# Performance work log

Measured on AMD Instinct MI355X. Metric: run time of the kernel, lower is better.

Reference implementation:

```python
import jax, jax.numpy as jnp
import numpy as np

NUM_HEADS = 32
NUM_KV_HEADS = 8
HEAD_DIM = 128
HIDDEN = 4096
ROPE_THETA = 10000.0
RMS_EPS = 1e-6


def setup_inputs() -> dict:
    key = jax.random.key(0)
    k1, k2, k3 = jax.random.split(key, 3)
    T = 2048
    qkv_out = (NUM_HEADS + 2 * NUM_KV_HEADS) * HEAD_DIM  # 6144
    return {
        "positions": jnp.arange(T, dtype=jnp.int64),
        "hidden_states": jax.random.normal(k1, (T, HIDDEN), dtype=jnp.float32),
        "wqkv": jax.random.normal(k2, (qkv_out, HIDDEN), dtype=jnp.float32) * 0.02,
        "wo": jax.random.normal(k3, (HIDDEN, NUM_HEADS * HEAD_DIM), dtype=jnp.float32) * 0.02,
        "q_norm_w": jnp.ones((HEAD_DIM,), dtype=jnp.float32),
        "k_norm_w": jnp.ones((HEAD_DIM,), dtype=jnp.float32),
    }


def _rms_norm(x, w):
    # per-head RMSNorm over last dim, computed in fp32 (matches Dots1RMSNorm)
    xf = x.astype(jnp.float32)
    var = jnp.mean(xf * xf, axis=-1, keepdims=True)
    return (w * (xf * jax.lax.rsqrt(var + RMS_EPS))).astype(x.dtype)


def _rope(x, positions):
    # NeoX-style rotary: rotate halves. x: [T, H, D]
    half = HEAD_DIM // 2
    inv_freq = 1.0 / (ROPE_THETA ** (jnp.arange(0, half, dtype=jnp.float32) / half))
    ang = positions.astype(jnp.float32)[:, None] * inv_freq  # [T, half]
    cos = jnp.cos(ang)[:, None, :]  # [T,1,half]
    sin = jnp.sin(ang)[:, None, :]
    x1, x2 = x[..., :half], x[..., half:]
    return jnp.concatenate([x1 * cos - x2 * sin, x2 * cos + x1 * sin], axis=-1)


def reference(positions, hidden_states, wqkv, wo, q_norm_w, k_norm_w):
    T = hidden_states.shape[0]
    q_size = NUM_HEADS * HEAD_DIM
    kv_size = NUM_KV_HEADS * HEAD_DIM
    qkv = hidden_states @ wqkv.T  # [T, q_size + 2*kv_size]
    q = qkv[:, :q_size].reshape(T, NUM_HEADS, HEAD_DIM)
    k = qkv[:, q_size:q_size + kv_size].reshape(T, NUM_KV_HEADS, HEAD_DIM)
    v = qkv[:, q_size + kv_size:].reshape(T, NUM_KV_HEADS, HEAD_DIM)

    q = _rms_norm(q, q_norm_w)
    k = _rms_norm(k, k_norm_w)
    q = _rope(q, positions)
    k = _rope(k, positions)

    # GQA: expand kv heads to query heads (group of 4)
    group = NUM_HEADS // NUM_KV_HEADS
    k = jnp.repeat(k, group, axis=1)  # [T, H, D]
    v = jnp.repeat(v, group, axis=1)

    scale = HEAD_DIM ** -0.5
    scores = jnp.einsum('thd,shd->hts', q, k) * scale  # [H, T, T]
    causal = positions[:, None] >= positions[None, :]
    scores = jnp.where(causal[None, :, :], scores, jnp.finfo(scores.dtype).min)
    probs = jax.nn.softmax(scores, axis=-1)
    attn = jnp.einsum('hts,shd->thd', probs, v)  # [T, H, D]
    out = attn.reshape(T, NUM_HEADS * HEAD_DIM) @ wo.T  # [T, HIDDEN]
    return out
```

## Files before the change

kernel.cpp:

```cpp
#include <hip/hip_runtime.h>


#define T_SEQ 2048
#define HID   4096
#define NH    32
#define NKVH  8
#define HD    128
#define QKVN  6144
#define QSZ   4096
#define QKN   5120

typedef unsigned short u16;
typedef __attribute__((ext_vector_type(8))) short short8;
typedef __attribute__((ext_vector_type(4))) float floatx4;

__device__ __forceinline__ float bf2f(u16 u) {
  union { unsigned int i; float f; } c; c.i = ((unsigned int)u) << 16; return c.f;
}
__device__ __forceinline__ u16 f2bf(float f) {
  union { float f; unsigned int i; } c; c.f = f;
  unsigned int u = c.i;
  return (u16)((u + 0x7FFFu + ((u >> 16) & 1u)) >> 16);
}
__device__ __forceinline__ floatx4 mfma16(short8 a, short8 b, floatx4 c) {
  return __builtin_amdgcn_mfma_f32_16x16x32_bf16(a, b, c, 0, 0, 0);
}

#define GLD16(g, l) __builtin_amdgcn_global_load_lds( \
    (__attribute__((address_space(1))) unsigned int*)(g), \
    (__attribute__((address_space(3))) unsigned int*)(l), 16, 0, 0)

__global__ __launch_bounds__(256) void cvt3_kernel(
    const float* __restrict__ s0, const float* __restrict__ s1,
    const float* __restrict__ s2, u16* __restrict__ d0, u16* __restrict__ d1,
    u16* __restrict__ d2, int n0, int n1, int n2) {
  int total = n0 + n1 + n2;
  int stride = gridDim.x * 256;
  for (int i = blockIdx.x * 256 + threadIdx.x; i < total; i += stride) {
    const float* s; u16* d; int j = i;
    if (j < n0)           { s = s0; d = d0; }
    else if (j < n0 + n1) { j -= n0; s = s1; d = d1; }
    else                  { j -= n0 + n1; s = s2; d = d2; }
    float4 a = ((const float4*)s)[2 * j];
    float4 b = ((const float4*)s)[2 * j + 1];
    union { ushort u[8]; uint4 v; } o;
    o.u[0] = f2bf(a.x); o.u[1] = f2bf(a.y); o.u[2] = f2bf(a.z); o.u[3] = f2bf(a.w);
    o.u[4] = f2bf(b.x); o.u[5] = f2bf(b.y); o.u[6] = f2bf(b.z); o.u[7] = f2bf(b.w);
    ((uint4*)d)[j] = o.v;
  }
}

template <int MODE>
__global__ __launch_bounds__(256, 2) void gemm_bt(const u16* __restrict__ A,
    const u16* __restrict__ B, void* __restrict__ Cv, u16* __restrict__ VT,
    int mtiles, int K, int ldC) {
  __shared__ __attribute__((aligned(16))) u16 As[128 * 64];
  __shared__ __attribute__((aligned(16))) u16 Bs[128 * 64];
  const int tid = threadIdx.x;
  const int wave = tid >> 6, lane = tid & 63;
  const int lq = lane >> 4, lc = lane & 15;
  const int wm = wave >> 1, wn = wave & 1;
  const int id = ((int)blockIdx.x & 7) * ((int)gridDim.x >> 3) + ((int)blockIdx.x >> 3);
  const int by = id % mtiles, bx = id / mtiles;
  const int m0 = by * 128, n0 = bx * 128;

  floatx4 acc[4][4];
#pragma unroll
  for (int i = 0; i < 4; ++i)
#pragma unroll
    for (int j = 0; j < 4; ++j) acc[i][j] = {0.f, 0.f, 0.f, 0.f};

  int arow[4], brow[4];
#pragma unroll
  for (int i = 0; i < 4; ++i) {
    arow[i] = wm * 64 + i * 16 + lc;
    brow[i] = wn * 64 + i * 16 + lc;
  }

  const u16* asrc[4]; const u16* bsrc[4];
#pragma unroll
  for (int r = 0; r < 4; ++r) {
    int L = r * 256 + tid;
    int mm = L >> 3;
    int cc = (L & 7) ^ (mm & 7);
    asrc[r] = A + (size_t)(m0 + mm) * K + cc * 8;
    bsrc[r] = B + (size_t)(n0 + mm) * K + cc * 8;
  }

  for (int k0 = 0; k0 < K; k0 += 64) {
#pragma unroll
    for (int r = 0; r < 4; ++r) {
      GLD16(asrc[r] + k0, As + (r * 256 + wave * 64) * 8);
      GLD16(bsrc[r] + k0, Bs + (r * 256 + wave * 64) * 8);
    }
    __syncthreads();
#pragma unroll
    for (int kb = 0; kb < 2; ++kb) {
      short8 af[4], bfr[4];
#pragma unroll
      for (int mi = 0; mi < 4; ++mi)
        af[mi] = *(const short8*)&As[arow[mi] * 64 + (((kb * 4 + lq) ^ (arow[mi] & 7)) * 8)];
#pragma unroll
      for (int ni = 0; ni < 4; ++ni)
        bfr[ni] = *(const short8*)&Bs[brow[ni] * 64 + (((kb * 4 + lq) ^ (brow[ni] & 7)) * 8)];
#pragma unroll
      for (int mi = 0; mi < 4; ++mi)
#pragma unroll
        for (int ni = 0; ni < 4; ++ni)
          acc[mi][ni] = mfma16(af[mi], bfr[ni], acc[mi][ni]);
    }
    __syncthreads();
  }

  if (MODE == 1 && n0 >= 5120) {
#pragma unroll
    for (int mi = 0; mi < 4; ++mi) {
      int row = m0 + wm * 64 + mi * 16 + lq * 4;
#pragma unroll
      for (int ni = 0; ni < 4; ++ni) {
        int rel = n0 + wn * 64 + ni * 16 + lc - 5120;
        ushort4 u;
        u.x = f2bf(acc[mi][ni][0]); u.y = f2bf(acc[mi][ni][1]);
        u.z = f2bf(acc[mi][ni][2]); u.w = f2bf(acc[mi][ni][3]);
        *(ushort4*)&VT[(size_t)rel * T_SEQ + row] = u;
      }
    }
  } else {
#pragma unroll
    for (int mi = 0; mi < 4; ++mi) {
      int row = m0 + wm * 64 + mi * 16 + lq * 4;
#pragma unroll
      for (int ni = 0; ni < 4; ++ni) {
        int col = n0 + wn * 64 + ni * 16 + lc;
#pragma unroll
        for (int r = 0; r < 4; ++r) {
          if (MODE == 1)
            ((u16*)Cv)[(size_t)(row + r) * ldC + col] = f2bf(acc[mi][ni][r]);
          else
            ((float*)Cv)[(size_t)(row + r) * ldC + col] = acc[mi][ni][r];
        }
      }
    }
  }
}

__global__ __launch_bounds__(256) void norm_rope_kernel(const u16* __restrict__ qk,
    const float* __restrict__ qw, const float* __restrict__ kw,
    u16* __restrict__ Qo, u16* __restrict__ Ko) {
  const int t = blockIdx.x;
  const int w = threadIdx.x >> 6;
  const int l = threadIdx.x & 63;
  const float inv = exp2f((float)l * -0.20762050593045158f);
  float s, c;
  __sincosf((float)t * inv, &s, &c);
  const float qwl = qw[l], qwh = qw[l + 64];
  const float kwl = kw[l], kwh = kw[l + 64];
  const u16* row = qk + (size_t)t * QKN;
#pragma unroll 2
  for (int hs = w; hs < NH + NKVH; hs += 4) {
    const bool isq = hs < NH;
    const u16* src = row + hs * HD;
    float x1 = bf2f(src[l]);
    float x2 = bf2f(src[l + 64]);
    float ss = x1 * x1 + x2 * x2;
#pragma unroll
    for (int m = 1; m < 64; m <<= 1) ss += __shfl_xor(ss, m);
    float rstd = rsqrtf(ss * (1.0f / HD) + 1e-6f);
    float n1 = x1 * rstd * (isq ? qwl : kwl);
    float n2 = x2 * rstd * (isq ? qwh : kwh);
    float o1 = n1 * c - n2 * s;
    float o2 = n2 * c + n1 * s;
    if (isq) {
      o1 *= 0.08838834764831845f; o2 *= 0.08838834764831845f;
      u16* dst = Qo + ((size_t)hs * T_SEQ + t) * HD;
      dst[l] = f2bf(o1); dst[l + 64] = f2bf(o2);
    } else {
      u16* dst = Ko + ((size_t)(hs - NH) * T_SEQ + t) * HD;
      dst[l] = f2bf(o1); dst[l + 64] = f2bf(o2);
    }
  }
}

__global__ __launch_bounds__(256, 2) void attn_kernel(const u16* __restrict__ Qg,
    const u16* __restrict__ Kg, const u16* __restrict__ VTg, u16* __restrict__ Og) {
  __shared__ __attribute__((aligned(16))) u16 Ks[8192];
  __shared__ __attribute__((aligned(16))) u16 Vs[2][8192];
  __shared__ __attribute__((aligned(16))) u16 Ps[8192];

  const int bid = blockIdx.x;
  const int h = bid & 31;
  const int qq = bid >> 5;
  const int qt = (qq < 8) ? (15 - qq) : (qq - 8);
  const int kvh = h >> 2;
  const int tid = threadIdx.x;
  const int wave = tid >> 6, lane = tid & 63;
  const int lq = lane >> 4, lc = lane & 15;

  const u16* kbase[4];
  const u16* vbase[4];
#pragma unroll
  for (int i = 0; i < 4; ++i) {
    int L = i * 256 + tid;
    int s = L >> 4, cp = L & 15;
    kbase[i] = Kg + ((size_t)kvh * T_SEQ + s) * HD + ((cp ^ (s & 15)) * 8);
    int d = L >> 3, cv = L & 7;
    vbase[i] = VTg + ((size_t)kvh * HD + d) * T_SEQ + ((cv ^ (d & 7)) * 8);
  }

  short8 qf[2][4];
#pragma unroll
  for (int mb = 0; mb < 2; ++mb)
#pragma unroll
    for (int ks = 0; ks < 4; ++ks) {
      int t = qt * 128 + wave * 32 + mb * 16 + lc;
      qf[mb][ks] = *(const short8*)&Qg[((size_t)h * T_SEQ + t) * HD + ks * 32 + lq * 8];
    }

  short8 ones;
#pragma unroll
  for (int j = 0; j < 8; ++j) ones[j] = (short)0x3F80;

  floatx4 of[2][8];
  floatx4 lacc[2];
#pragma unroll
  for (int mb = 0; mb < 2; ++mb) {
    lacc[mb] = {0.f, 0.f, 0.f, 0.f};
#pragma unroll
    for (int db = 0; db < 8; ++db) of[mb][db] = {0.f, 0.f, 0.f, 0.f};
  }

  const int ktmax = 2 * qt + 1;
  const int t0g = qt * 128 + wave * 32;
  const int wave_tmax = t0g + 31;

#pragma unroll
  for (int i = 0; i < 4; ++i) {
    GLD16(kbase[i], Ks + (i * 256 + wave * 64) * 8);
    GLD16(vbase[i], Vs[0] + (i * 256 + wave * 64) * 8);
  }

  for (int kt = 0; kt <= ktmax; ++kt) {
    __syncthreads();
    if (kt + 1 <= ktmax) {
      u16* vd = Vs[(kt + 1) & 1] + (size_t)wave * 64 * 8;
#pragma unroll
      for (int i = 0; i < 4; ++i)
        GLD16(vbase[i] + (kt + 1) * 64, vd + i * 256 * 8);
    }
    const bool active = (kt * 64) <= wave_tmax;
    if (active) {
      floatx4 sf[2][4];
#pragma unroll
      for (int mb = 0; mb < 2; ++mb)
#pragma unroll
        for (int nb = 0; nb < 4; ++nb) sf[mb][nb] = {0.f, 0.f, 0.f, 0.f};
#pragma unroll
      for (int ks = 0; ks < 4; ++ks) {
        short8 kf[4];
#pragma unroll
        for (int nb = 0; nb < 4; ++nb)
          kf[nb] = *(const short8*)&Ks[(nb * 16 + lc) * 128 + ((4 * ks + lq) ^ lc) * 8];
#pragma unroll
        for (int mb = 0; mb < 2; ++mb)
#pragma unroll
          for (int nb = 0; nb < 4; ++nb)
            sf[mb][nb] = mfma16(kf[nb], qf[mb][ks], sf[mb][nb]);
      }
      const bool nm = (kt * 64 + 63) > t0g;
#pragma unroll
      for (int mb = 0; mb < 2; ++mb) {
        const int trow = wave * 32 + mb * 16 + lc;
        const int tg = qt * 128 + trow;
#pragma unroll
        for (int nb = 0; nb < 4; ++nb) {
          ushort4 u;
          float p0 = __expf(sf[mb][nb][0]);
          float p1 = __expf(sf[mb][nb][1]);
          float p2 = __expf(sf[mb][nb][2]);
          float p3 = __expf(sf[mb][nb][3]);
          if (nm) {
            int sg = kt * 64 + nb * 16 + lq * 4;
            p0 = (sg + 0 <= tg) ? p0 : 0.f;
            p1 = (sg + 1 <= tg) ? p1 : 0.f;
            p2 = (sg + 2 <= tg) ? p2 : 0.f;
            p3 = (sg + 3 <= tg) ? p3 : 0.f;
          }
          u.x = f2bf(p0); u.y = f2bf(p1); u.z = f2bf(p2); u.w = f2bf(p3);
          int c = 2 * nb + (lq >> 1);
          *(ushort4*)&Ps[trow * 64 + ((c ^ (trow & 7)) * 8) + (lq & 1) * 4] = u;
        }
      }
    }
    __syncthreads();
    if (kt + 1 <= ktmax) {
      u16* kd = Ks + (size_t)wave * 64 * 8;
#pragma unroll
      for (int i = 0; i < 4; ++i)
        GLD16(kbase[i] + (size_t)(kt + 1) * 8192, kd + i * 256 * 8);
    }
    if (active) {
      const u16* vb = Vs[kt & 1];
      short8 pf[2][2];
#pragma unroll
      for (int mb = 0; mb < 2; ++mb)
#pragma unroll
        for (int k2 = 0; k2 < 2; ++k2) {
          int trow = wave * 32 + mb * 16 + lc;
          pf[mb][k2] =
              *(const short8*)&Ps[trow * 64 + (((4 * k2 + lq) ^ (lc & 7)) * 8)];
        }
#pragma unroll
      for (int k2 = 0; k2 < 2; ++k2) {
#pragma unroll
        for (int db = 0; db < 8; ++db) {
          short8 vf =
              *(const short8*)&vb[(db * 16 + lc) * 64 + (((4 * k2 + lq) ^ (lc & 7)) * 8)];
          of[0][db] = mfma16(pf[0][k2], vf, of[0][db]);
          of[1][db] = mfma16(pf[1][k2], vf, of[1][db]);
        }
        lacc[0] = mfma16(pf[0][k2], ones, lacc[0]);
        lacc[1] = mfma16(pf[1][k2], ones, lacc[1]);
      }
    }
  }
#pragma unroll
  for (int mb = 0; mb < 2; ++mb)
#pragma unroll
    for (int r = 0; r < 4; ++r) {
      float inv = 1.f / lacc[mb][r];
      int tg = qt * 128 + wave * 32 + mb * 16 + lq * 4 + r;
#pragma unroll
      for (int db = 0; db < 8; ++db)
        Og[(size_t)tg * QSZ + h * HD + db * 16 + lc] = f2bf(of[mb][db][r] * inv);
    }
}

extern "C" void kernel_launch(void* const* d_in, const int* in_sizes, int n_in,
                              void* d_out, int out_size, void* d_ws, size_t ws_size,
                              hipStream_t stream) {
  (void)in_sizes; (void)n_in; (void)out_size; (void)ws_size;
  const float* hidden = (const float*)d_in[1];
  const float* wqkv   = (const float*)d_in[2];
  const float* wo     = (const float*)d_in[3];
  const float* qw     = (const float*)d_in[4];
  const float* kw     = (const float*)d_in[5];
  float* out = (float*)d_out;
  char* ws = (char*)d_ws;

  u16* h_bf    = (u16*)(ws + 0);
  u16* wq_bf   = (u16*)(ws + 16777216);
  u16* wo_bf   = (u16*)(ws + 67108864);
  u16* vT_bf   = (u16*)(ws + 100663296);
  u16* qk_bf   = (u16*)(ws + 104857600);
  u16* q_bf    = (u16*)(ws + 16777216);
  u16* k_bf    = (u16*)(ws + 33554432);
  u16* attn_bf = (u16*)(ws + 0);

  cvt3_kernel<<<4096, 256, 0, stream>>>(
      hidden, wqkv, wo, h_bf, wq_bf, wo_bf,
      T_SEQ * HID / 8, QKVN * HID / 8, HID * QSZ / 8);

  gemm_bt<1><<<768, 256, 0, stream>>>(h_bf, wq_bf, qk_bf, vT_bf,
                                      T_SEQ / 128, HID, QKN);

  norm_rope_kernel<<<T_SEQ, 256, 0, stream>>>(qk_bf, qw, kw, q_bf, k_bf);

  attn_kernel<<<512, 256, 0, stream>>>(q_bf, k_bf, vT_bf, attn_bf);

  gemm_bt<0><<<512, 256, 0, stream>>>(attn_bf, wo_bf, out, vT_bf,
                                      T_SEQ / 128, HID, QSZ);
}
```

Baseline: 471.8 us.

## Double-buffer K tiles in attention and vectorize norm/rope kernel

The attention kernel now keeps two K tiles in LDS, so the next K tile is prefetched together with the next V tile at the top of each iteration. Previously the K load could only start after the mid-iteration barrier. The norm/rope kernel is also rewritten so each lane handles 4 contiguous elements with vector loads and stores, and two heads are processed per wave. The rotary partner values are exchanged with a lane shuffle. The extra 16KB of LDS per block may lower occupancy on the attention kernel, which has launch bounds of 2 blocks per CU.

```diff
diff --git a/kernel.cpp b/kernel.cpp
--- a/kernel.cpp
+++ b/kernel.cpp
@@ -150,40 +150,66 @@
   const int t = blockIdx.x;
   const int w = threadIdx.x >> 6;
   const int l = threadIdx.x & 63;
-  const float inv = exp2f((float)l * -0.20762050593045158f);
-  float s, c;
-  __sincosf((float)t * inv, &s, &c);
-  const float qwl = qw[l], qwh = qw[l + 64];
-  const float kwl = kw[l], kwh = kw[l + 64];
+  const int half = l >> 5;
+  const int d0 = (l & 31) * 4;
+  const int fi = d0 & 63;
+  float c4[4], s4[4];
+#pragma unroll
+  for (int j = 0; j < 4; ++j) {
+    float invf = exp2f((float)(fi + j) * -0.20762050593045158f);
+    __sincosf((float)t * invf, &s4[j], &c4[j]);
+  }
+  const bool hi = (d0 >= 64);
   const u16* row = qk + (size_t)t * QKN;
-#pragma unroll 2
-  for (int hs = w; hs < NH + NKVH; hs += 4) {
-    const bool isq = hs < NH;
-    const u16* src = row + hs * HD;
-    float x1 = bf2f(src[l]);
-    float x2 = bf2f(src[l + 64]);
-    float ss = x1 * x1 + x2 * x2;
-#pragma unroll
-    for (int m = 1; m < 64; m <<= 1) ss += __shfl_xor(ss, m);
+#pragma unroll
+  for (int it = 0; it < 5; ++it) {
+    const int p = w * 2 + it * 8;
+    const int hs = p + half;
+    const bool isq = p < NH;
+    const float* wptr = isq ? qw : kw;
+    float4 wv = *(const float4*)(wptr + d0);
+    ushort4 xv = *(const ushort4*)(row + hs * HD + d0);
+    float x0 = bf2f(xv.x), x1 = bf2f(xv.y), x2 = bf2f(xv.z), x3 = bf2f(xv.w);
+    float ss = x0 * x0 + x1 * x1 + x2 * x2 + x3 * x3;
+#pragma unroll
+    for (int m = 1; m < 32; m <<= 1) ss += __shfl_xor(ss, m);
     float rstd = rsqrtf(ss * (1.0f / HD) + 1e-6f);
-    float n1 = x1 * rstd * (isq ? qwl : kwl);
-    float n2 = x2 * rstd * (isq ? qwh : kwh);
-    float o1 = n1 * c - n2 * s;
-    float o2 = n2 * c + n1 * s;
+    float n0 = x0 * rstd * wv.x;
+    float n1 = x1 * rstd * wv.y;
+    float n2 = x2 * rstd * wv.z;
+    float n3 = x3 * rstd * wv.w;
+    float p0 = __shfl_xor(n0, 16);
+    float p1 = __shfl_xor(n1, 16);
+    float p2 = __shfl_xor(n2, 16);
+    float p3 = __shfl_xor(n3, 16);
+    float o0, o1, o2, o3;
+    if (!hi) {
+      o0 = n0 * c4[0] - p0 * s4[0];
+      o1 = n1 * c4[1] - p1 * s4[1];
+      o2 = n2 * c4[2] - p2 * s4[2];
+      o3 = n3 * c4[3] - p3 * s4[3];
+    } else {
+      o0 = n0 * c4[0] + p0 * s4[0];
+      o1 = n1 * c4[1] + p1 * s4[1];
+      o2 = n2 * c4[2] + p2 * s4[2];
+      o3 = n3 * c4[3] + p3 * s4[3];
+    }
+    ushort4 ov;
     if (isq) {
-      o1 *= 0.08838834764831845f; o2 *= 0.08838834764831845f;
-      u16* dst = Qo + ((size_t)hs * T_SEQ + t) * HD;
-      dst[l] = f2bf(o1); dst[l + 64] = f2bf(o2);
+      const float sc = 0.08838834764831845f;
+      ov.x = f2bf(o0 * sc); ov.y = f2bf(o1 * sc);
+      ov.z = f2bf(o2 * sc); ov.w = f2bf(o3 * sc);
+      *(ushort4*)(Qo + ((size_t)hs * T_SEQ + t) * HD + d0) = ov;
     } else {
-      u16* dst = Ko + ((size_t)(hs - NH) * T_SEQ + t) * HD;
-      dst[l] = f2bf(o1); dst[l + 64] = f2bf(o2);
+      ov.x = f2bf(o0); ov.y = f2bf(o1); ov.z = f2bf(o2); ov.w = f2bf(o3);
+      *(ushort4*)(Ko + ((size_t)(hs - NH) * T_SEQ + t) * HD + d0) = ov;
     }
   }
 }
 
 __global__ __launch_bounds__(256, 2) void attn_kernel(const u16* __restrict__ Qg,
     const u16* __restrict__ Kg, const u16* __restrict__ VTg, u16* __restrict__ Og) {
-  __shared__ __attribute__((aligned(16))) u16 Ks[8192];
+  __shared__ __attribute__((aligned(16))) u16 Ks[2][8192];
   __shared__ __attribute__((aligned(16))) u16 Vs[2][8192];
   __shared__ __attribute__((aligned(16))) u16 Ps[8192];
 
@@ -235,7 +261,7 @@
 
 #pragma unroll
   for (int i = 0; i < 4; ++i) {
-    GLD16(kbase[i], Ks + (i * 256 + wave * 64) * 8);
+    GLD16(kbase[i], Ks[0] + (i * 256 + wave * 64) * 8);
     GLD16(vbase[i], Vs[0] + (i * 256 + wave * 64) * 8);
   }
 
@@ -243,9 +269,12 @@
     __syncthreads();
     if (kt + 1 <= ktmax) {
       u16* vd = Vs[(kt + 1) & 1] + (size_t)wave * 64 * 8;
-#pragma unroll
-      for (int i = 0; i < 4; ++i)
+      u16* kd = Ks[(kt + 1) & 1] + (size_t)wave * 64 * 8;
+#pragma unroll
+      for (int i = 0; i < 4; ++i) {
         GLD16(vbase[i] + (kt + 1) * 64, vd + i * 256 * 8);
+        GLD16(kbase[i] + (size_t)(kt + 1) * 8192, kd + i * 256 * 8);
+      }
     }
     const bool active = (kt * 64) <= wave_tmax;
     if (active) {
@@ -254,12 +283,13 @@
       for (int mb = 0; mb < 2; ++mb)
 #pragma unroll
         for (int nb = 0; nb < 4; ++nb) sf[mb][nb] = {0.f, 0.f, 0.f, 0.f};
+      const u16* kb = Ks[kt & 1];
 #pragma unroll
       for (int ks = 0; ks < 4; ++ks) {
         short8 kf[4];
 #pragma unroll
         for (int nb = 0; nb < 4; ++nb)
-          kf[nb] = *(const short8*)&Ks[(nb * 16 + lc) * 128 + ((4 * ks + lq) ^ lc) * 8];
+          kf[nb] = *(const short8*)&kb[(nb * 16 + lc) * 128 + ((4 * ks + lq) ^ lc) * 8];
 #pragma unroll
         for (int mb = 0; mb < 2; ++mb)
 #pragma unroll
@@ -292,12 +322,6 @@
       }
     }
     __syncthreads();
-    if (kt + 1 <= ktmax) {
-      u16* kd = Ks + (size_t)wave * 64 * 8;
-#pragma unroll
-      for (int i = 0; i < 4; ++i)
-        GLD16(kbase[i] + (size_t)(kt + 1) * 8192, kd + i * 256 * 8);
-    }
     if (active) {
       const u16* vb = Vs[kt & 1];
       short8 pf[2][2];
```

Measured after the change: 484.1 us. 2.6% more time.
